# Kernel optimization log

Hardware: AMD Instinct MI355X
Metric: run time of the kernel (lower is better)

## Reference

```python
import jax, jax.numpy as jnp
import numpy as np

OBS, HID, LAT = 1024, 2048, 256
VOCAB, HQ = 8192, 4
COMMIT = 0.5
N = 16384
LN_EPS = 1e-5


def setup_inputs() -> dict:
    key = jax.random.key(0)
    ks = jax.random.split(key, 7)

    def lin_w(k, fan_in, shape):
        # torch nn.Linear default init: U(-1/sqrt(fan_in), 1/sqrt(fan_in))
        bound = 1.0 / np.sqrt(fan_in)
        return jax.random.uniform(k, shape, jnp.float32, -bound, bound)

    return {
        "x": jax.random.normal(ks[0], (N, OBS), jnp.float32),
        # embeddings initialized uniform(-0.5, 0.5) as in the module
        "codebooks": jax.random.uniform(ks[1], (HQ, VOCAB, LAT), jnp.float32, -0.5, 0.5),
        "enc_w1": lin_w(ks[2], OBS, (OBS, HID)),
        "enc_b1": jnp.zeros((HID,), jnp.float32),
        "ln_g": jnp.ones((HID,), jnp.float32),
        "ln_b": jnp.zeros((HID,), jnp.float32),
        "enc_w2": lin_w(ks[3], HID, (HID, LAT)),
        "enc_b2": jnp.zeros((LAT,), jnp.float32),
        "dec_w1": lin_w(ks[4], LAT, (LAT, HID)),
        "dec_b1": jnp.zeros((HID,), jnp.float32),
        "dec_w2": lin_w(ks[5], HID, (HID, OBS)),
        "dec_b2": jnp.zeros((OBS,), jnp.float32),
    }


def reference(x, codebooks, enc_w1, enc_b1, ln_g, ln_b, enc_w2, enc_b2,
              dec_w1, dec_b1, dec_w2, dec_b2):
    sg = jax.lax.stop_gradient
    # encoder: Linear -> LayerNorm -> ReLU -> Linear
    h = x @ enc_w1 + enc_b1                      # [N, HID]
    mu = h.mean(-1, keepdims=True)
    var = ((h - mu) ** 2).mean(-1, keepdims=True)  # biased var, matches torch LN
    h = (h - mu) * jax.lax.rsqrt(var + LN_EPS) * ln_g + ln_b
    h = jax.nn.relu(h)
    latent = h @ enc_w2 + enc_b2                 # [N, LAT]

    total = jnp.float32(0.0)
    resid = latent
    code_sum = jnp.zeros_like(latent)
    for l in range(HQ):
        E = codebooks[l]                         # [VOCAB, LAT]
        # squared euclidean distances (argmin identical to cdist argmin)
        d2 = ((resid * resid).sum(-1, keepdims=True)
              - 2.0 * (resid @ E.T)
              + (E * E).sum(-1))                 # [N, VOCAB]
        idx = jnp.argmin(d2, axis=-1)            # [N]
        q = E[idx]                               # [N, LAT] gather
        codebook_loss = jnp.mean((q - sg(resid)) ** 2)
        commit_loss = jnp.mean((sg(q) - resid) ** 2)
        total = total + codebook_loss + COMMIT * commit_loss
        code_sum = code_sum + q
        resid = resid - q

    # straight-through estimator
    quant = latent + sg(code_sum - latent)
    # decoder: Linear -> ReLU -> Linear
    dh = jax.nn.relu(quant @ dec_w1 + dec_b1)
    recon = dh @ dec_w2 + dec_b2                 # [N, OBS]
    total = total + 0.5 * jnp.mean((recon - x) ** 2)
    return total
```

## Files before the change

kernel.cpp:

```cpp
#include <hip/hip_runtime.h>

#define N_ROWS 16384
#define OBS    1024
#define HID    2048
#define LAT    256
#define VOCAB  8192
#define HQ     4
#define LN_EPS 1e-5f

typedef unsigned short u16;
typedef unsigned long long u64;
typedef __bf16 bf16x8 __attribute__((ext_vector_type(8)));
typedef float  f32x4  __attribute__((ext_vector_type(4)));

static __device__ __forceinline__ unsigned int float_to_ordered(float f) {
    unsigned int u = __float_as_uint(f);
    return (u & 0x80000000u) ? ~u : (u | 0x80000000u);
}
static __device__ __forceinline__ u16 f2bf(float f) {
    unsigned int u = __float_as_uint(f);
    unsigned int r = u + 0x7FFFu + ((u >> 16) & 1u);
    return (u16)(r >> 16);
}
static __device__ __forceinline__ float bf2f(u16 u) {
    return __uint_as_float((unsigned int)u << 16);
}

#define GL2LDS(gp, lp) __builtin_amdgcn_global_load_lds( \
    (const __attribute__((address_space(1))) void*)(gp), \
    (__attribute__((address_space(3))) void*)(lp), 16, 0, 0)

template<int EPI>
__global__ __launch_bounds__(256, 4) void mfma_gemm_k(
    const u16* __restrict__ Abf, const u16* __restrict__ Bbf,
    const float* __restrict__ bias,
    u16* __restrict__ Cbf,
    const float* __restrict__ X, double* __restrict__ lacc,
    int K, int Nd)
{
    __shared__ u16 As[128 * 64];
    __shared__ u16 Bs[128 * 64];

    const int tid  = threadIdx.x;
    const int wv   = tid >> 6, lane = tid & 63;
    const int wm   = wv & 1,   wn   = wv >> 1;
    const int m_   = lane & 15, g   = lane >> 4;
    const int m0   = blockIdx.x * 128;
    const int n0   = blockIdx.y * 128;

    f32x4 acc[4][4];
#pragma unroll
    for (int i = 0; i < 4; ++i)
#pragma unroll
        for (int j = 0; j < 4; ++j)
            acc[i][j] = f32x4{0.f, 0.f, 0.f, 0.f};

    const u16* Ablk = Abf + (size_t)m0 * K;
    const u16* Bblk = Bbf + (size_t)n0 * K;

    for (int k0 = 0; k0 < K; k0 += 64) {
#pragma unroll
        for (int c = 0; c < 4; ++c) {
            const int ci = (wv * 4 + c) * 64 + lane;
            const int r  = ci >> 3;
            const int cc = ci & 7;
            const int kc = (cc ^ (r & 7)) << 3;
            GL2LDS(Ablk + (size_t)r * K + k0 + kc, As + (wv * 4 + c) * 512);
            GL2LDS(Bblk + (size_t)r * K + k0 + kc, Bs + (wv * 4 + c) * 512);
        }
        __syncthreads();
#pragma unroll
        for (int ks = 0; ks < 2; ++ks) {
            const int ccw = ks * 4 + g;
            const int sw  = (ccw ^ (m_ & 7)) << 3;
            bf16x8 af[4], bfr[4];
#pragma unroll
            for (int t = 0; t < 4; ++t) {
                af[t]  = *(const bf16x8*)&As[(wm * 64 + t * 16 + m_) * 64 + sw];
                bfr[t] = *(const bf16x8*)&Bs[(wn * 64 + t * 16 + m_) * 64 + sw];
            }
#pragma unroll
            for (int mi = 0; mi < 4; ++mi)
#pragma unroll
                for (int ni = 0; ni < 4; ++ni)
                    acc[mi][ni] = __builtin_amdgcn_mfma_f32_16x16x32_bf16(
                        af[mi], bfr[ni], acc[mi][ni], 0, 0, 0);
        }
        __syncthreads();
    }

    float bs[4];
#pragma unroll
    for (int ni = 0; ni < 4; ++ni) bs[ni] = bias[n0 + wn * 64 + ni * 16 + m_];

    if constexpr (EPI == 3) {
        float lsum = 0.f;
#pragma unroll
        for (int mi = 0; mi < 4; ++mi)
#pragma unroll
            for (int j = 0; j < 4; ++j) {
                const int row = m0 + wm * 64 + mi * 16 + g * 4 + j;
#pragma unroll
                for (int ni = 0; ni < 4; ++ni) {
                    const int col = n0 + wn * 64 + ni * 16 + m_;
                    float r = acc[mi][ni][j] + bs[ni] - X[(size_t)row * Nd + col];
                    lsum = fmaf(r, r, lsum);
                }
            }
#pragma unroll
        for (int off = 32; off >= 1; off >>= 1) lsum += __shfl_xor(lsum, off);
        __shared__ float red[4];
        if (lane == 0) red[wv] = lsum;
        __syncthreads();
        if (tid == 0)
            atomicAdd(lacc, (double)(red[0] + red[1] + red[2] + red[3]));
    } else {
#pragma unroll
        for (int mi = 0; mi < 4; ++mi)
#pragma unroll
            for (int j = 0; j < 4; ++j) {
                const int row = m0 + wm * 64 + mi * 16 + g * 4 + j;
#pragma unroll
                for (int ni = 0; ni < 4; ++ni) {
                    const int col = n0 + wn * 64 + ni * 16 + m_;
                    float v = acc[mi][ni][j] + bs[ni];
                    if constexpr (EPI == 1) v = fmaxf(v, 0.f);
                    Cbf[(size_t)row * Nd + col] = f2bf(v);
                }
            }
    }
}

__global__ __launch_bounds__(256, 4) void gemm2_k(
    const u16* __restrict__ Abf, const u16* __restrict__ Bbf,
    const float* __restrict__ bias,
    float* __restrict__ lat, float* __restrict__ resid, u16* __restrict__ rbf)
{
    __shared__ u16 As[64 * 64];
    __shared__ u16 Bs[64 * 64];

    const int tid = threadIdx.x;
    const int wv  = tid >> 6, lane = tid & 63;
    const int wm  = wv & 1,   wn   = wv >> 1;
    const int m_  = lane & 15, g   = lane >> 4;
    const int m0  = blockIdx.x * 64;
    const int n0  = blockIdx.y * 64;

    f32x4 acc[2][2];
#pragma unroll
    for (int i = 0; i < 2; ++i)
#pragma unroll
        for (int j = 0; j < 2; ++j)
            acc[i][j] = f32x4{0.f, 0.f, 0.f, 0.f};

    const u16* Ablk = Abf + (size_t)m0 * HID;
    const u16* Bblk = Bbf + (size_t)n0 * HID;

    for (int k0 = 0; k0 < HID; k0 += 64) {
#pragma unroll
        for (int c = 0; c < 2; ++c) {
            const int ci = (wv * 2 + c) * 64 + lane;
            const int r  = ci >> 3;
            const int cc = ci & 7;
            const int kc = (cc ^ (r & 7)) << 3;
            GL2LDS(Ablk + (size_t)r * HID + k0 + kc, As + (wv * 2 + c) * 512);
            GL2LDS(Bblk + (size_t)r * HID + k0 + kc, Bs + (wv * 2 + c) * 512);
        }
        __syncthreads();
#pragma unroll
        for (int ks = 0; ks < 2; ++ks) {
            const int ccw = ks * 4 + g;
            const int sw  = (ccw ^ (m_ & 7)) << 3;
            bf16x8 af[2], bfr[2];
#pragma unroll
            for (int t = 0; t < 2; ++t) {
                af[t]  = *(const bf16x8*)&As[(wm * 32 + t * 16 + m_) * 64 + sw];
                bfr[t] = *(const bf16x8*)&Bs[(wn * 32 + t * 16 + m_) * 64 + sw];
            }
#pragma unroll
            for (int mi = 0; mi < 2; ++mi)
#pragma unroll
                for (int ni = 0; ni < 2; ++ni)
                    acc[mi][ni] = __builtin_amdgcn_mfma_f32_16x16x32_bf16(
                        af[mi], bfr[ni], acc[mi][ni], 0, 0, 0);
        }
        __syncthreads();
    }

#pragma unroll
    for (int mi = 0; mi < 2; ++mi)
#pragma unroll
        for (int j = 0; j < 4; ++j) {
            const int row = m0 + wm * 32 + mi * 16 + g * 4 + j;
#pragma unroll
            for (int ni = 0; ni < 2; ++ni) {
                const int col = n0 + wn * 32 + ni * 16 + m_;
                float v = acc[mi][ni][j] + bias[col];
                lat  [(size_t)row * LAT + col] = v;
                resid[(size_t)row * LAT + col] = v;
                rbf  [(size_t)row * LAT + col] = f2bf(v);
            }
        }
}

__global__ __launch_bounds__(256) void tpose4_k(
    const float* __restrict__ W0, u16* __restrict__ T0,
    const float* __restrict__ W1, u16* __restrict__ T1,
    const float* __restrict__ W2, u16* __restrict__ T2,
    const float* __restrict__ W3, u16* __restrict__ T3)
{
    __shared__ u16 t[32][33];
    const int bid = blockIdx.x;
    const float* W; u16* T; int K, N, r;
    if (bid < 2048)      { W = W0; T = T0; K = OBS; N = HID; r = bid; }
    else if (bid < 2560) { W = W1; T = T1; K = HID; N = LAT; r = bid - 2048; }
    else if (bid < 3072) { W = W2; T = T2; K = LAT; N = HID; r = bid - 2560; }
    else                 { W = W3; T = T3; K = HID; N = OBS; r = bid - 3072; }
    const int nb = N >> 5;
    const int n0 = (r % nb) * 32, k0 = (r / nb) * 32;
    const int lx = threadIdx.x & 31, ly = threadIdx.x >> 5;
#pragma unroll
    for (int i = 0; i < 4; ++i)
        t[ly + 8 * i][lx] = f2bf(W[(size_t)(k0 + ly + 8 * i) * N + n0 + lx]);
    __syncthreads();
#pragma unroll
    for (int i = 0; i < 4; ++i)
        T[(size_t)(n0 + ly + 8 * i) * K + k0 + lx] = t[lx][ly + 8 * i];
}

__device__ __forceinline__ float block_reduce_bcast(float v, float* scratch) {
#pragma unroll
    for (int off = 32; off >= 1; off >>= 1) v += __shfl_xor(v, off);
    const int tid = threadIdx.x;
    __syncthreads();
    if ((tid & 63) == 0) scratch[tid >> 6] = v;
    __syncthreads();
    return scratch[0] + scratch[1] + scratch[2] + scratch[3];
}

__global__ __launch_bounds__(256) void ln_relu_bf_k(
    u16* __restrict__ h, const float* __restrict__ g, const float* __restrict__ b)
{
    __shared__ float scratch[4];
    const int tid = threadIdx.x;
    u16* hp = h + (size_t)blockIdx.x * HID + tid * 8;

    ushort4 r0 = *(const ushort4*)hp;
    ushort4 r1 = *(const ushort4*)(hp + 4);
    float v[8] = {bf2f(r0.x), bf2f(r0.y), bf2f(r0.z), bf2f(r0.w),
                  bf2f(r1.x), bf2f(r1.y), bf2f(r1.z), bf2f(r1.w)};

    float s = 0.f;
#pragma unroll
    for (int e = 0; e < 8; ++e) s += v[e];
    const float mu = block_reduce_bcast(s, scratch) * (1.f / HID);

    float vs = 0.f;
#pragma unroll
    for (int e = 0; e < 8; ++e) { float d = v[e] - mu; vs = fmaf(d, d, vs); }
    const float var = block_reduce_bcast(vs, scratch) * (1.f / HID);
    const float rs = rsqrtf(var + LN_EPS);

    ushort4 o0, o1;
#pragma unroll
    for (int e = 0; e < 8; ++e) {
        const int col = tid * 8 + e;
        float w = (v[e] - mu) * rs * g[col] + b[col];
        w = fmaxf(w, 0.f);
        u16 bb = f2bf(w);
        if (e < 4) ((u16*)&o0)[e] = bb; else ((u16*)&o1)[e - 4] = bb;
    }
    *(ushort4*)hp = o0;
    *(ushort4*)(hp + 4) = o1;
}

__global__ __launch_bounds__(256) void enorm_k(
    const float* __restrict__ cb, float* __restrict__ enorm,
    u16* __restrict__ cbb, u64* __restrict__ keys, double* __restrict__ accs)
{
    if (blockIdx.x < 64) keys[blockIdx.x * 256 + threadIdx.x] = ~0ull;
    if (blockIdx.x == 64 && threadIdx.x < 2) accs[threadIdx.x] = 0.0;
    const int row  = blockIdx.x * 4 + (threadIdx.x >> 6);
    const int lane = threadIdx.x & 63;
    const size_t off = (size_t)row * LAT + lane * 4;
    float4 v = *(const float4*)(cb + off);
    ushort4 o;
    o.x = f2bf(-2.f * v.x); o.y = f2bf(-2.f * v.y);
    o.z = f2bf(-2.f * v.z); o.w = f2bf(-2.f * v.w);
    *(ushort4*)(cbb + off) = o;
    float s = v.x * v.x + v.y * v.y + v.z * v.z + v.w * v.w;
#pragma unroll
    for (int off2 = 32; off2 >= 1; off2 >>= 1) s += __shfl_xor(s, off2);
    if (lane == 0) enorm[row] = s;
}

__global__ __launch_bounds__(256) void f2bf_k(
    const float* __restrict__ in, u16* __restrict__ out)
{
    size_t i = ((size_t)blockIdx.x * 256 + threadIdx.x) * 4;
    float4 v = *(const float4*)(in + i);
    ushort4 o;
    o.x = f2bf(v.x); o.y = f2bf(v.y); o.z = f2bf(v.z); o.w = f2bf(v.w);
    *(ushort4*)(out + i) = o;
}

__global__ __launch_bounds__(256, 4) void dist_mfma_k(
    const u16* __restrict__ Abf, const u16* __restrict__ Bneg2,
    const float* __restrict__ enorm, u64* __restrict__ keys)
{
    __shared__ u16 As[128 * 64];
    __shared__ u16 Bs[128 * 64];
    __shared__ u64 shk[128][2];

    const int tid  = threadIdx.x;
    const int wv   = tid >> 6, lane = tid & 63;
    const int wm   = wv & 1,   wn   = wv >> 1;
    const int m_   = lane & 15, g   = lane >> 4;
    const int m0   = blockIdx.x * 128;
    const int n0   = blockIdx.y * 128;

    f32x4 acc[4][4];
#pragma unroll
    for (int ni = 0; ni < 4; ++ni) {
        const float en = enorm[n0 + wn * 64 + ni * 16 + m_];
#pragma unroll
        for (int mi = 0; mi < 4; ++mi)
            acc[mi][ni] = f32x4{en, en, en, en};
    }

    const u16* Ablk = Abf   + (size_t)m0 * LAT;
    const u16* Bblk = Bneg2 + (size_t)n0 * LAT;

    for (int k0 = 0; k0 < LAT; k0 += 64) {
#pragma unroll
        for (int c = 0; c < 4; ++c) {
            const int ci = (wv * 4 + c) * 64 + lane;
            const int r  = ci >> 3;
            const int cc = ci & 7;
            const int kc = (cc ^ (r & 7)) << 3;
            GL2LDS(Ablk + (size_t)r * LAT + k0 + kc, As + (wv * 4 + c) * 512);
            GL2LDS(Bblk + (size_t)r * LAT + k0 + kc, Bs + (wv * 4 + c) * 512);
        }
        __syncthreads();
#pragma unroll
        for (int ks = 0; ks < 2; ++ks) {
            const int ccw = ks * 4 + g;
            const int sw  = (ccw ^ (m_ & 7)) << 3;
            bf16x8 af[4], bfr[4];
#pragma unroll
            for (int t = 0; t < 4; ++t) {
                af[t]  = *(const bf16x8*)&As[(wm * 64 + t * 16 + m_) * 64 + sw];
                bfr[t] = *(const bf16x8*)&Bs[(wn * 64 + t * 16 + m_) * 64 + sw];
            }
#pragma unroll
            for (int mi = 0; mi < 4; ++mi)
#pragma unroll
                for (int ni = 0; ni < 4; ++ni)
                    acc[mi][ni] = __builtin_amdgcn_mfma_f32_16x16x32_bf16(
                        af[mi], bfr[ni], acc[mi][ni], 0, 0, 0);
        }
        __syncthreads();
    }

#pragma unroll
    for (int mi = 0; mi < 4; ++mi)
#pragma unroll
        for (int j = 0; j < 4; ++j) {
            float bs_ = acc[mi][0][j];
            int   bi_ = n0 + wn * 64 + m_;
#pragma unroll
            for (int ni = 1; ni < 4; ++ni) {
                const float s = acc[mi][ni][j];
                const int   v = n0 + wn * 64 + ni * 16 + m_;
                if (s < bs_) { bs_ = s; bi_ = v; }
            }
            u64 best = ((u64)float_to_ordered(bs_) << 32) | (unsigned)bi_;
#pragma unroll
            for (int mask = 1; mask <= 8; mask <<= 1) {
                u64 o = __shfl_xor(best, mask);
                best = o < best ? o : best;
            }
            if (m_ == 0) shk[wm * 64 + mi * 16 + g * 4 + j][wn] = best;
        }
    __syncthreads();
    if (tid < 128) {
        u64 a = shk[tid][0], b = shk[tid][1];
        atomicMin(&keys[m0 + tid], a < b ? a : b);
    }
}

template<bool LAST>
__global__ __launch_bounds__(256) void vq_update_k(
    float* __restrict__ resid, u16* __restrict__ aux,
    const float* __restrict__ latent,
    const float* __restrict__ E,
    u64* __restrict__ keys, double* __restrict__ acc)
{
    __shared__ float red[4];
    const int tid = threadIdx.x;
    const int base = blockIdx.x * 16;
    float lsum = 0.f;
    for (int r = 0; r < 16; ++r) {
        const int row = base + r;
        const int idx = (int)(keys[row] & 0xFFFFFFFFull);
        const float q = E[(size_t)idx * LAT + tid];
        float v = resid[(size_t)row * LAT + tid] - q;
        if constexpr (LAST) {
            aux[(size_t)row * LAT + tid] =
                f2bf(latent[(size_t)row * LAT + tid] - v);
        } else {
            resid[(size_t)row * LAT + tid] = v;
            aux[(size_t)row * LAT + tid] = f2bf(v);
        }
        lsum = fmaf(v, v, lsum);
    }
    if (!LAST && tid < 16) keys[base + tid] = ~0ull;
#pragma unroll
    for (int off = 32; off >= 1; off >>= 1) lsum += __shfl_xor(lsum, off);
    if ((tid & 63) == 0) red[tid >> 6] = lsum;
    __syncthreads();
    if (tid == 0) atomicAdd(acc, (double)(red[0] + red[1] + red[2] + red[3]));
}

__global__ void finalize_k(const double* __restrict__ acc, float* __restrict__ out) {
    double total = 1.5 * acc[0] / (double)((size_t)N_ROWS * LAT)
                 + 0.5 * acc[1] / (double)((size_t)N_ROWS * OBS);
    out[0] = (float)total;
}

extern "C" void kernel_launch(void* const* d_in, const int* in_sizes, int n_in,
                              void* d_out, int out_size, void* d_ws, size_t ws_size,
                              hipStream_t stream)
{
    const float* x      = (const float*)d_in[0];
    const float* cb     = (const float*)d_in[1];
    const float* enc_w1 = (const float*)d_in[2];
    const float* enc_b1 = (const float*)d_in[3];
    const float* ln_g   = (const float*)d_in[4];
    const float* ln_b   = (const float*)d_in[5];
    const float* enc_w2 = (const float*)d_in[6];
    const float* enc_b2 = (const float*)d_in[7];
    const float* dec_w1 = (const float*)d_in[8];
    const float* dec_b1 = (const float*)d_in[9];
    const float* dec_w2 = (const float*)d_in[10];
    const float* dec_b2 = (const float*)d_in[11];

    char* ws = (char*)d_ws;
    const size_t MB = 1ull << 20;
    u16* hbuf = (u16*)ws;
    u16* cbb  = (u16*)(ws + 64 * MB);
    u16* rbf  = (u16*)(ws + 80 * MB);
    u16* qbf  = (u16*)(ws + 88 * MB);
    u16* xbf  = (u16*)(ws + 96 * MB);
    float* latent = (float*)(ws + 96 * MB);
    float* resid  = (float*)(ws + 112 * MB);
    u16* w1T  = (u16*)(ws + 128 * MB);
    u16* w2T  = (u16*)(ws + 132 * MB);
    u16* wd1T = (u16*)(ws + 133 * MB);
    u16* wd2T = (u16*)(ws + 134 * MB);
    float* enorm = (float*)(ws + 138 * MB);
    u64*   keys  = (u64*)(ws + 138 * MB + 131072);
    double* accs = (double*)(ws + 138 * MB + 262144);

    enorm_k<<<HQ * VOCAB / 4, 256, 0, stream>>>(cb, enorm, cbb, keys, accs);

    tpose4_k<<<5120, 256, 0, stream>>>(enc_w1, w1T, enc_w2, w2T,
                                       dec_w1, wd1T, dec_w2, wd2T);
    f2bf_k<<<(int)((size_t)N_ROWS * OBS / 1024), 256, 0, stream>>>(x, xbf);

    mfma_gemm_k<0><<<dim3(N_ROWS / 128, HID / 128), 256, 0, stream>>>(
        xbf, w1T, enc_b1, hbuf, nullptr, nullptr, OBS, HID);
    ln_relu_bf_k<<<N_ROWS, 256, 0, stream>>>(hbuf, ln_g, ln_b);
    gemm2_k<<<dim3(N_ROWS / 64, LAT / 64), 256, 0, stream>>>(
        hbuf, w2T, enc_b2, latent, resid, rbf);

    for (int l = 0; l < HQ; ++l) {
        dist_mfma_k<<<dim3(N_ROWS / 128, VOCAB / 128), 256, 0, stream>>>(
            rbf, cbb + (size_t)l * VOCAB * LAT, enorm + (size_t)l * VOCAB, keys);
        if (l < HQ - 1)
            vq_update_k<false><<<N_ROWS / 16, 256, 0, stream>>>(
                resid, rbf, nullptr, cb + (size_t)l * VOCAB * LAT, keys, accs);
        else
            vq_update_k<true><<<N_ROWS / 16, 256, 0, stream>>>(
                resid, qbf, latent, cb + (size_t)l * VOCAB * LAT, keys, accs);
    }

    mfma_gemm_k<1><<<dim3(N_ROWS / 128, HID / 128), 256, 0, stream>>>(
        qbf, wd1T, dec_b1, hbuf, nullptr, nullptr, LAT, HID);
    mfma_gemm_k<3><<<dim3(N_ROWS / 128, OBS / 128), 256, 0, stream>>>(
        hbuf, wd2T, dec_b2, nullptr, x, accs + 1, HID, OBS);

    finalize_k<<<1, 1, 0, stream>>>(accs, (float*)d_out);
}
```

Before: 891.1 us.

## Fuse VQ residual update into distance kernel via last-block completion counter

Removes the separate vq_update kernel launch at each quantizer level. Each distance block now increments a per-row-tile atomic counter after its atomicMin. The last of the 64 vocab blocks for that tile reads the final argmin keys, gathers the codebook rows, updates resid and the bf16 buffer, accumulates the loss and resets the keys. This saves launch and inter-kernel gaps. The cost is a __threadfence, the extra counter atomics, and a serial 128-row update tail running in only one block per row tile.

```diff
diff --git a/kernel.cpp b/kernel.cpp
--- a/kernel.cpp
+++ b/kernel.cpp
@@ -276,10 +276,13 @@
 
 __global__ __launch_bounds__(256) void enorm_k(
     const float* __restrict__ cb, float* __restrict__ enorm,
-    u16* __restrict__ cbb, u64* __restrict__ keys, double* __restrict__ accs)
+    u16* __restrict__ cbb, u64* __restrict__ keys, double* __restrict__ accs,
+    int* __restrict__ cnt)
 {
     if (blockIdx.x < 64) keys[blockIdx.x * 256 + threadIdx.x] = ~0ull;
     if (blockIdx.x == 64 && threadIdx.x < 2) accs[threadIdx.x] = 0.0;
+    if (blockIdx.x == 65) cnt[threadIdx.x] = 0;
+    if (blockIdx.x == 66) cnt[256 + threadIdx.x] = 0;
     const int row  = blockIdx.x * 4 + (threadIdx.x >> 6);
     const int lane = threadIdx.x & 63;
     const size_t off = (size_t)row * LAT + lane * 4;
@@ -304,13 +307,20 @@
     *(ushort4*)(out + i) = o;
 }
 
+template<bool LAST>
 __global__ __launch_bounds__(256, 4) void dist_mfma_k(
     const u16* __restrict__ Abf, const u16* __restrict__ Bneg2,
-    const float* __restrict__ enorm, u64* __restrict__ keys)
+    const float* __restrict__ enorm, u64* __restrict__ keys,
+    float* __restrict__ resid, u16* __restrict__ aux,
+    const float* __restrict__ latent, const float* __restrict__ Ecb,
+    int* __restrict__ cnt, double* __restrict__ accs)
 {
     __shared__ u16 As[128 * 64];
     __shared__ u16 Bs[128 * 64];
     __shared__ u64 shk[128][2];
+    __shared__ int sidx[128];
+    __shared__ int sflag;
+    __shared__ float red[4];
 
     const int tid  = threadIdx.x;
     const int wv   = tid >> 6, lane = tid & 63;
@@ -387,23 +397,22 @@
         u64 a = shk[tid][0], b = shk[tid][1];
         atomicMin(&keys[m0 + tid], a < b ? a : b);
     }
-}
-
-template<bool LAST>
-__global__ __launch_bounds__(256) void vq_update_k(
-    float* __restrict__ resid, u16* __restrict__ aux,
-    const float* __restrict__ latent,
-    const float* __restrict__ E,
-    u64* __restrict__ keys, double* __restrict__ acc)
-{
-    __shared__ float red[4];
-    const int tid = threadIdx.x;
-    const int base = blockIdx.x * 16;
+    __threadfence();
+    __syncthreads();
+    if (tid == 0) sflag = atomicAdd(&cnt[blockIdx.x], 1);
+    __syncthreads();
+    if (sflag != 63) return;
+
+    if (tid < 128) {
+        u64 k = atomicAdd(&keys[m0 + tid], 0ull);
+        sidx[tid] = (int)(k & 0xFFFFFFFFull);
+        if (!LAST) keys[m0 + tid] = ~0ull;
+    }
+    __syncthreads();
     float lsum = 0.f;
-    for (int r = 0; r < 16; ++r) {
-        const int row = base + r;
-        const int idx = (int)(keys[row] & 0xFFFFFFFFull);
-        const float q = E[(size_t)idx * LAT + tid];
+    for (int r = 0; r < 128; ++r) {
+        const int row = m0 + r;
+        const float q = Ecb[(size_t)sidx[r] * LAT + tid];
         float v = resid[(size_t)row * LAT + tid] - q;
         if constexpr (LAST) {
             aux[(size_t)row * LAT + tid] =
@@ -414,12 +423,12 @@
         }
         lsum = fmaf(v, v, lsum);
     }
-    if (!LAST && tid < 16) keys[base + tid] = ~0ull;
 #pragma unroll
     for (int off = 32; off >= 1; off >>= 1) lsum += __shfl_xor(lsum, off);
     if ((tid & 63) == 0) red[tid >> 6] = lsum;
     __syncthreads();
-    if (tid == 0) atomicAdd(acc, (double)(red[0] + red[1] + red[2] + red[3]));
+    if (tid == 0)
+        atomicAdd(accs, (double)(red[0] + red[1] + red[2] + red[3]));
 }
 
 __global__ void finalize_k(const double* __restrict__ acc, float* __restrict__ out) {
@@ -461,8 +470,9 @@
     float* enorm = (float*)(ws + 138 * MB);
     u64*   keys  = (u64*)(ws + 138 * MB + 131072);
     double* accs = (double*)(ws + 138 * MB + 262144);
-
-    enorm_k<<<HQ * VOCAB / 4, 256, 0, stream>>>(cb, enorm, cbb, keys, accs);
+    int*   cnt   = (int*)(ws + 138 * MB + 262144 + 4096);
+
+    enorm_k<<<HQ * VOCAB / 4, 256, 0, stream>>>(cb, enorm, cbb, keys, accs, cnt);
 
     tpose4_k<<<5120, 256, 0, stream>>>(enc_w1, w1T, enc_w2, w2T,
                                        dec_w1, wd1T, dec_w2, wd2T);
@@ -475,14 +485,16 @@
         hbuf, w2T, enc_b2, latent, resid, rbf);
 
     for (int l = 0; l < HQ; ++l) {
-        dist_mfma_k<<<dim3(N_ROWS / 128, VOCAB / 128), 256, 0, stream>>>(
-            rbf, cbb + (size_t)l * VOCAB * LAT, enorm + (size_t)l * VOCAB, keys);
+        const u16*   Bn = cbb + (size_t)l * VOCAB * LAT;
+        const float* en = enorm + (size_t)l * VOCAB;
+        const float* E  = cb + (size_t)l * VOCAB * LAT;
+        int* cl = cnt + l * 128;
         if (l < HQ - 1)
-            vq_update_k<false><<<N_ROWS / 16, 256, 0, stream>>>(
-                resid, rbf, nullptr, cb + (size_t)l * VOCAB * LAT, keys, accs);
+            dist_mfma_k<false><<<dim3(N_ROWS / 128, VOCAB / 128), 256, 0, stream>>>(
+                rbf, Bn, en, keys, resid, rbf, nullptr, E, cl, accs);
         else
-            vq_update_k<true><<<N_ROWS / 16, 256, 0, stream>>>(
-                resid, qbf, latent, cb + (size_t)l * VOCAB * LAT, keys, accs);
+            dist_mfma_k<true><<<dim3(N_ROWS / 128, VOCAB / 128), 256, 0, stream>>>(
+                rbf, Bn, en, keys, resid, qbf, latent, E, cl, accs);
     }
 
     mfma_gemm_k<1><<<dim3(N_ROWS / 128, HID / 128), 256, 0, stream>>>(
```

Result: slower. 2.657 ms (+198.2%).
